# Optimization experiments

Hardware: AMD Instinct MI355X
Metric: run time of the kernel (lower is better)

## Reference

```python
import jax, jax.numpy as jnp
import numpy as np

B, S, D_MODEL, D_K, D_V = 4, 2048, 1024, 1024, 1024


def setup_inputs() -> dict:
    key = jax.random.key(0)
    k1, k2, k3, k4 = jax.random.split(key, 4)
    scale = 1.0 / np.sqrt(D_MODEL)
    x = jax.random.normal(k1, (B, S, D_MODEL), dtype=jnp.float32)
    Wq = jax.random.normal(k2, (D_K, D_MODEL), dtype=jnp.float32) * scale
    Wk = jax.random.normal(k3, (D_K, D_MODEL), dtype=jnp.float32) * scale
    Wv = jax.random.normal(k4, (D_V, D_MODEL), dtype=jnp.float32) * scale
    # causal mask: position i may attend to j <= i (True = keep)
    mask = jnp.broadcast_to(jnp.tril(jnp.ones((S, S), dtype=bool)), (B, S, S))
    return {"x": x, "mask": mask, "Wq": Wq, "Wk": Wk, "Wv": Wv}


def reference(x, mask, Wq, Wk, Wv):
    # nn.Linear(d, k, bias=False): y = x @ W.T with W of shape [k, d]
    q = jnp.einsum('bsd,kd->bsk', x, Wq)
    k = jnp.einsum('bsd,kd->bsk', x, Wk)
    v = jnp.einsum('bsd,vd->bsv', x, Wv)
    scores = jnp.einsum('bik,bjk->bij', q, k) / jnp.sqrt(jnp.float32(D_K))
    s = jnp.where(mask, scores, -jnp.inf)
    # masked, fully-masked-row-safe softmax (fully masked rows -> all zeros,
    # matching softmax[all-masked rows] = 0 in the original)
    m = jnp.max(s, axis=-1, keepdims=True)
    m_safe = jnp.where(jnp.isfinite(m), m, 0.0)
    e = jnp.exp(s - m_safe)          # exp(-inf) = 0 for masked entries
    denom = jnp.sum(e, axis=-1, keepdims=True)
    p = e / jnp.where(denom == 0.0, 1.0, denom)
    return jnp.einsum('bij,bjv->biv', p, v)
```

## Files before the change

### kernel.cpp

```cpp
#include <hip/hip_runtime.h>
#include <hip/hip_bf16.h>
#include <stdint.h>

#define SEQ   2048
#define DM    1024
#define NBAT  4

typedef __attribute__((ext_vector_type(8))) short  short8;
typedef __attribute__((ext_vector_type(4))) float  floatx4;

__device__ __forceinline__ unsigned short f2b(float f) {
    __hip_bfloat16 h = __float2bfloat16(f);
    unsigned short r;
    __builtin_memcpy(&r, &h, 2);
    return r;
}

__device__ __forceinline__ ushort4 pack4(float a, float b, float c, float d) {
    ushort4 u; u.x = f2b(a); u.y = f2b(b); u.z = f2b(c); u.w = f2b(d); return u;
}

__device__ __forceinline__ void gload16(const void* g, void* s) {
    __builtin_amdgcn_global_load_lds(
        (const __attribute__((address_space(1))) unsigned int*)(uintptr_t)g,
        (__attribute__((address_space(3))) unsigned int*)(uintptr_t)s,
        16, 0, 0);
}

__global__ void prep(const float4* __restrict__ x,
                     const float4* __restrict__ w0, const float4* __restrict__ w1,
                     const float4* __restrict__ w2,
                     ushort4* __restrict__ xb, ushort4* __restrict__ wall,
                     float* __restrict__ rsum)
{
    const int b = blockIdx.x;
    const int t = threadIdx.x;
    if (b < 8192) {
        const int i = b * 256 + t;
        float4 f = x[i];
        xb[i] = pack4(f.x, f.y, f.z, f.w);
    } else if (b < 11264) {
        const int idx  = b - 8192;
        const int wsel = idx >> 10;
        const int i    = (idx & 1023) * 256 + t;
        const float4* src = (wsel == 0) ? w0 : (wsel == 1) ? w1 : w2;
        float4 f = src[i];
        wall[(size_t)wsel * 262144 + i] = pack4(f.x, f.y, f.z, f.w);
    } else {
        rsum[(b - 11264) * 256 + t] = 0.f;
    }
}

template<int EPI>
__global__ __launch_bounds__(512, 2) void gemm256(
    const unsigned short* __restrict__ Ag, const unsigned short* __restrict__ Bg,
    void* __restrict__ P0, void* __restrict__ P1, void* __restrict__ P2,
    float* __restrict__ rowsum, float qscale)
{
    __shared__ __align__(16) unsigned short lds[65536];

    int m0, n0, ntl = 0, z = 0;
    const unsigned short* A;
    const unsigned short* Bm;

    if (EPI == 0) {
        const int bid = blockIdx.x;
        const int wg  = (bid & 7) * 48 + (bid >> 3);
        const int mt  = wg / 12; ntl = wg - mt * 12;
        m0 = mt * 256; n0 = ntl * 256;
        A = Ag; Bm = Bg;
    } else {
        z = blockIdx.z;
        const int f = blockIdx.x;
        int ti = (int)((sqrtf(8.f * f + 1.f) - 1.f) * 0.5f);
        while ((ti + 1) * (ti + 2) / 2 <= f) ti++;
        while (ti * (ti + 1) / 2 > f) ti--;
        const int tj = f - ti * (ti + 1) / 2;
        m0 = ti * 256; n0 = tj * 256;
        A = Ag + (size_t)z * SEQ * DM; Bm = Bg + (size_t)z * SEQ * DM;
    }

    const int t    = threadIdx.x;
    const int w    = t >> 6;
    const int lane = t & 63;
    const int wr   = w >> 2, wc = w & 3;
    const int r    = lane & 15, q = lane >> 4;

    const int srow = lane >> 3;
    const int scol = ((lane & 7) ^ srow) << 3;

    const int sk0 = ((0 + q) ^ (r & 7)) * 8;
    const int sk1 = ((4 + q) ^ (r & 7)) * 8;
    const int aRd = wr * 8192 + r * 64;
    const int bRd = 16384 + (wc >> 1) * 8192 + ((wc & 1) * 64 + r) * 64;

    floatx4 acc[8][4];
#pragma unroll
    for (int i = 0; i < 8; i++)
#pragma unroll
        for (int j = 0; j < 4; j++)
            acc[i][j] = (floatx4){0.f, 0.f, 0.f, 0.f};

#define STGC(G, R0, KB, CB) do { \
    gload16((G) + (size_t)((R0) + w * 16 + srow)     * DM + (KB) + scol, &lds[(CB) + w * 1024]); \
    gload16((G) + (size_t)((R0) + w * 16 + srow + 8) * DM + (KB) + scol, &lds[(CB) + w * 1024 + 512]); \
  } while (0)
#define STG4(KB, OB) do { \
    STGC(A,  m0,       (KB), (OB)); \
    STGC(A,  m0 + 128, (KB), (OB) + 8192); \
    STGC(Bm, n0,       (KB), (OB) + 16384); \
    STGC(Bm, n0 + 128, (KB), (OB) + 24576); \
  } while (0)

#define ONE_MFMA(AC, AF, BF) do { \
    if (EPI == 0) (AC) = __builtin_amdgcn_mfma_f32_16x16x32_bf16((AF), (BF), (AC), 0, 0, 0); \
    else          (AC) = __builtin_amdgcn_mfma_f32_16x16x32_bf16((BF), (AF), (AC), 0, 0, 0); \
  } while (0)

    STG4(0, 0);

    for (int tt = 0; tt < 16; ++tt) {
        const int cb  = (tt & 1) * 32768;
        const int ob  = 32768 - cb;
        const int nkb = (tt + 1 < 16 ? tt + 1 : 0) * 64;

        asm volatile("s_waitcnt vmcnt(0)" ::: "memory");
        __builtin_amdgcn_s_barrier();

        short8 a0[8], b0[4];
#pragma unroll
        for (int i = 0; i < 8; i++)
            a0[i] = *(const short8*)&lds[cb + aRd + i * 1024 + sk0];
#pragma unroll
        for (int j = 0; j < 4; j++)
            b0[j] = *(const short8*)&lds[cb + bRd + j * 1024 + sk0];

        STG4(nkb, ob);

        __builtin_amdgcn_s_setprio(1);
#pragma unroll
        for (int i = 0; i < 8; i++)
#pragma unroll
            for (int j = 0; j < 4; j++)
                ONE_MFMA(acc[i][j], a0[i], b0[j]);

        short8 a1[8], b1[4];
#pragma unroll
        for (int i = 0; i < 8; i++)
            a1[i] = *(const short8*)&lds[cb + aRd + i * 1024 + sk1];
#pragma unroll
        for (int j = 0; j < 4; j++)
            b1[j] = *(const short8*)&lds[cb + bRd + j * 1024 + sk1];
#pragma unroll
        for (int i = 0; i < 8; i++)
#pragma unroll
            for (int j = 0; j < 4; j++)
                ONE_MFMA(acc[i][j], a1[i], b1[j]);
        __builtin_amdgcn_s_setprio(0);
    }
#undef STGC
#undef STG4
#undef ONE_MFMA

    if (EPI == 0) {
        const int gmb = m0 + wr * 128 + q * 4;
        const int gnb = n0 + wc * 64 + r;
        unsigned short* Qo  = (unsigned short*)P0;
        unsigned short* Ko  = (unsigned short*)P1;
        unsigned short* Vto = (unsigned short*)P2;
        if (ntl < 4) {
#pragma unroll
            for (int i = 0; i < 8; i++) {
                const int gm = gmb + i * 16;
#pragma unroll
                for (int j = 0; j < 4; j++) {
                    const int gn = gnb + j * 16;
#pragma unroll
                    for (int rr = 0; rr < 4; rr++)
                        Qo[(size_t)(gm + rr) * 1024 + gn] = f2b(acc[i][j][rr] * qscale);
                }
            }
        } else if (ntl < 8) {
#pragma unroll
            for (int i = 0; i < 8; i++) {
                const int gm = gmb + i * 16;
#pragma unroll
                for (int j = 0; j < 4; j++) {
                    const int gn = gnb + j * 16;
#pragma unroll
                    for (int rr = 0; rr < 4; rr++)
                        Ko[(size_t)(gm + rr) * 1024 + (gn - 1024)] = f2b(acc[i][j][rr]);
                }
            }
        } else {
#pragma unroll
            for (int i = 0; i < 8; i++) {
                const int gm = gmb + i * 16;
                const int b  = gm >> 11;
                const int s  = gm & 2047;
#pragma unroll
                for (int j = 0; j < 4; j++) {
                    const int v = gnb + j * 16 - 2048;
                    *(ushort4*)&Vto[((size_t)(b * 1024 + v)) * 2048 + s] =
                        pack4(acc[i][j][0], acc[i][j][1], acc[i][j][2], acc[i][j][3]);
                }
            }
        }
    } else {
        const int gmb = m0 + wr * 128 + r;
        const int gnb = n0 + wc * 64 + q * 4;
        unsigned short* E = (unsigned short*)P0 + (size_t)z * SEQ * SEQ;
        float* rs = rowsum + (size_t)z * SEQ;
#pragma unroll
        for (int i = 0; i < 8; i++) {
            const int gm = gmb + i * 16;
            float part = 0.f;
#pragma unroll
            for (int j = 0; j < 4; j++) {
                const int gn = gnb + j * 16;
                float e0 = (gn + 0 <= gm) ? __expf(acc[i][j][0]) : 0.f;
                float e1 = (gn + 1 <= gm) ? __expf(acc[i][j][1]) : 0.f;
                float e2 = (gn + 2 <= gm) ? __expf(acc[i][j][2]) : 0.f;
                float e3 = (gn + 3 <= gm) ? __expf(acc[i][j][3]) : 0.f;
                part += (e0 + e1) + (e2 + e3);
                *(ushort4*)&E[(size_t)gm * SEQ + gn] = pack4(e0, e1, e2, e3);
            }
            part += __shfl_xor(part, 16, 64);
            part += __shfl_xor(part, 32, 64);
            if (q == 0) atomicAdd(&rs[gm], part);
        }
    }
}

#define SLOTS 24576

__global__ __launch_bounds__(512, 2) void attn_pv(
    const unsigned short* __restrict__ Ag, const unsigned short* __restrict__ Bg,
    float* __restrict__ Cv, const float* __restrict__ rowsum)
{
    __shared__ __align__(16) unsigned short lds[3 * SLOTS];

    const int z = blockIdx.z;
    const int m0 = (int)(gridDim.y - 1 - blockIdx.y) * 256;
    const int n0 = blockIdx.x * 128;

    const unsigned short* A  = Ag + (size_t)z * SEQ * SEQ;
    const unsigned short* Bm = Bg + (size_t)z * DM * SEQ;
    const int NT = (m0 + 256) / 64;

    const int t    = threadIdx.x;
    const int w    = t >> 6;
    const int lane = t & 63;
    const int wr   = w >> 1, wc = w & 1;
    const int r    = lane & 15, q = lane >> 4;

    const int srow = lane >> 3;
    const int scol = ((lane & 7) ^ srow) << 3;

    const int aoff = (wr >> 1) * 8192 + ((wr & 1) * 64 + r) * 64;
    const int boff = 16384 + (wc * 64 + r) * 64;
    const int sk0  = ((0 + q) ^ (r & 7)) * 8;
    const int sk1  = ((4 + q) ^ (r & 7)) * 8;

    floatx4 acc[4][4];
#pragma unroll
    for (int i = 0; i < 4; i++)
#pragma unroll
        for (int j = 0; j < 4; j++)
            acc[i][j] = (floatx4){0.f, 0.f, 0.f, 0.f};

#define ASTG(KB, SL) do { \
    gload16(A + (size_t)(m0 +       w * 16 + srow) * SEQ + (KB) + scol, &lds[(SL) +         w * 1024]); \
    gload16(A + (size_t)(m0 +   8 + w * 16 + srow) * SEQ + (KB) + scol, &lds[(SL) +         w * 1024 + 512]); \
    gload16(A + (size_t)(m0 + 128 + w * 16 + srow) * SEQ + (KB) + scol, &lds[(SL) + 8192 +  w * 1024]); \
    gload16(A + (size_t)(m0 + 136 + w * 16 + srow) * SEQ + (KB) + scol, &lds[(SL) + 8192 +  w * 1024 + 512]); \
  } while (0)
#define BSTG(KB, SL) do { \
    gload16(Bm + (size_t)(n0 +      w * 16 + srow) * SEQ + (KB) + scol, &lds[(SL) + 16384 + w * 1024]); \
    gload16(Bm + (size_t)(n0 +  8 + w * 16 + srow) * SEQ + (KB) + scol, &lds[(SL) + 16384 + w * 1024 + 512]); \
  } while (0)

    ASTG(0, 0);
    BSTG(0, 0);
    ASTG(64, SLOTS);
    BSTG(64, SLOTS);
    asm volatile("s_waitcnt vmcnt(6)" ::: "memory");
    __builtin_amdgcn_s_barrier();

    for (int tt = 0; tt < NT; ++tt) {
        const int sl  = (tt % 3) * SLOTS;
        const int nsl = ((tt + 2) % 3) * SLOTS;
        const int nkb = (tt + 2 < NT) ? (tt + 2) * 64 : 0;

        const int aB = sl + aoff;
        const int bB = sl + boff;
        short8 a00 = *(const short8*)&lds[aB + sk0 +    0];
        short8 a10 = *(const short8*)&lds[aB + sk0 + 1024];
        short8 a20 = *(const short8*)&lds[aB + sk0 + 2048];
        short8 a30 = *(const short8*)&lds[aB + sk0 + 3072];
        short8 b00 = *(const short8*)&lds[bB + sk0 +    0];
        short8 b10 = *(const short8*)&lds[bB + sk0 + 1024];
        short8 b20 = *(const short8*)&lds[bB + sk0 + 2048];
        short8 b30 = *(const short8*)&lds[bB + sk0 + 3072];
        short8 a01 = *(const short8*)&lds[aB + sk1 +    0];
        short8 a11 = *(const short8*)&lds[aB + sk1 + 1024];
        short8 a21 = *(const short8*)&lds[aB + sk1 + 2048];
        short8 a31 = *(const short8*)&lds[aB + sk1 + 3072];
        short8 b01 = *(const short8*)&lds[bB + sk1 +    0];
        short8 b11 = *(const short8*)&lds[bB + sk1 + 1024];
        short8 b21 = *(const short8*)&lds[bB + sk1 + 2048];
        short8 b31 = *(const short8*)&lds[bB + sk1 + 3072];

        ASTG(nkb, nsl);
        BSTG(nkb, nsl);
        asm volatile("s_waitcnt vmcnt(6)" ::: "memory");
        __builtin_amdgcn_s_barrier();

        __builtin_amdgcn_s_setprio(1);
        acc[0][0] = __builtin_amdgcn_mfma_f32_16x16x32_bf16(b00, a00, acc[0][0], 0, 0, 0);
        acc[0][1] = __builtin_amdgcn_mfma_f32_16x16x32_bf16(b10, a00, acc[0][1], 0, 0, 0);
        acc[0][2] = __builtin_amdgcn_mfma_f32_16x16x32_bf16(b20, a00, acc[0][2], 0, 0, 0);
        acc[0][3] = __builtin_amdgcn_mfma_f32_16x16x32_bf16(b30, a00, acc[0][3], 0, 0, 0);
        acc[1][0] = __builtin_amdgcn_mfma_f32_16x16x32_bf16(b00, a10, acc[1][0], 0, 0, 0);
        acc[1][1] = __builtin_amdgcn_mfma_f32_16x16x32_bf16(b10, a10, acc[1][1], 0, 0, 0);
        acc[1][2] = __builtin_amdgcn_mfma_f32_16x16x32_bf16(b20, a10, acc[1][2], 0, 0, 0);
        acc[1][3] = __builtin_amdgcn_mfma_f32_16x16x32_bf16(b30, a10, acc[1][3], 0, 0, 0);
        acc[2][0] = __builtin_amdgcn_mfma_f32_16x16x32_bf16(b00, a20, acc[2][0], 0, 0, 0);
        acc[2][1] = __builtin_amdgcn_mfma_f32_16x16x32_bf16(b10, a20, acc[2][1], 0, 0, 0);
        acc[2][2] = __builtin_amdgcn_mfma_f32_16x16x32_bf16(b20, a20, acc[2][2], 0, 0, 0);
        acc[2][3] = __builtin_amdgcn_mfma_f32_16x16x32_bf16(b30, a20, acc[2][3], 0, 0, 0);
        acc[3][0] = __builtin_amdgcn_mfma_f32_16x16x32_bf16(b00, a30, acc[3][0], 0, 0, 0);
        acc[3][1] = __builtin_amdgcn_mfma_f32_16x16x32_bf16(b10, a30, acc[3][1], 0, 0, 0);
        acc[3][2] = __builtin_amdgcn_mfma_f32_16x16x32_bf16(b20, a30, acc[3][2], 0, 0, 0);
        acc[3][3] = __builtin_amdgcn_mfma_f32_16x16x32_bf16(b30, a30, acc[3][3], 0, 0, 0);
        acc[0][0] = __builtin_amdgcn_mfma_f32_16x16x32_bf16(b01, a01, acc[0][0], 0, 0, 0);
        acc[0][1] = __builtin_amdgcn_mfma_f32_16x16x32_bf16(b11, a01, acc[0][1], 0, 0, 0);
        acc[0][2] = __builtin_amdgcn_mfma_f32_16x16x32_bf16(b21, a01, acc[0][2], 0, 0, 0);
        acc[0][3] = __builtin_amdgcn_mfma_f32_16x16x32_bf16(b31, a01, acc[0][3], 0, 0, 0);
        acc[1][0] = __builtin_amdgcn_mfma_f32_16x16x32_bf16(b01, a11, acc[1][0], 0, 0, 0);
        acc[1][1] = __builtin_amdgcn_mfma_f32_16x16x32_bf16(b11, a11, acc[1][1], 0, 0, 0);
        acc[1][2] = __builtin_amdgcn_mfma_f32_16x16x32_bf16(b21, a11, acc[1][2], 0, 0, 0);
        acc[1][3] = __builtin_amdgcn_mfma_f32_16x16x32_bf16(b31, a11, acc[1][3], 0, 0, 0);
        acc[2][0] = __builtin_amdgcn_mfma_f32_16x16x32_bf16(b01, a21, acc[2][0], 0, 0, 0);
        acc[2][1] = __builtin_amdgcn_mfma_f32_16x16x32_bf16(b11, a21, acc[2][1], 0, 0, 0);
        acc[2][2] = __builtin_amdgcn_mfma_f32_16x16x32_bf16(b21, a21, acc[2][2], 0, 0, 0);
        acc[2][3] = __builtin_amdgcn_mfma_f32_16x16x32_bf16(b31, a21, acc[2][3], 0, 0, 0);
        acc[3][0] = __builtin_amdgcn_mfma_f32_16x16x32_bf16(b01, a31, acc[3][0], 0, 0, 0);
        acc[3][1] = __builtin_amdgcn_mfma_f32_16x16x32_bf16(b11, a31, acc[3][1], 0, 0, 0);
        acc[3][2] = __builtin_amdgcn_mfma_f32_16x16x32_bf16(b21, a31, acc[3][2], 0, 0, 0);
        acc[3][3] = __builtin_amdgcn_mfma_f32_16x16x32_bf16(b31, a31, acc[3][3], 0, 0, 0);
        __builtin_amdgcn_s_setprio(0);
    }
#undef ASTG
#undef BSTG

    const int gmb = m0 + wr * 64 + r;
    const int gnb = n0 + wc * 64 + q * 4;
    float* C = Cv + (size_t)z * SEQ * DM;
    const float* rs = rowsum + (size_t)z * SEQ;
#pragma unroll
    for (int i = 0; i < 4; i++) {
        const int gm = gmb + i * 16;
        const float inv = 1.0f / rs[gm];
#pragma unroll
        for (int j = 0; j < 4; j++) {
            const int gn = gnb + j * 16;
            float4 o;
            o.x = acc[i][j][0] * inv;
            o.y = acc[i][j][1] * inv;
            o.z = acc[i][j][2] * inv;
            o.w = acc[i][j][3] * inv;
            *(float4*)&C[(size_t)gm * DM + gn] = o;
        }
    }
}

extern "C" void kernel_launch(void* const* d_in, const int* in_sizes, int n_in,
                              void* d_out, int out_size, void* d_ws, size_t ws_size,
                              hipStream_t stream) {
    (void)in_sizes; (void)n_in; (void)out_size; (void)ws_size;
    const float* x  = (const float*)d_in[0];
    const float* Wq = (const float*)d_in[2];
    const float* Wk = (const float*)d_in[3];
    const float* Wv = (const float*)d_in[4];

    char* base = (char*)d_ws;
    size_t off = 0;
    auto alloc = [&](size_t n) { char* p = base + off; off += (n + 255) & ~(size_t)255; return p; };

    unsigned short* xb   = (unsigned short*)alloc((size_t)NBAT * SEQ * DM * 2);
    unsigned short* wall = (unsigned short*)alloc((size_t)3 * DM * DM * 2);
    unsigned short* Qb   = (unsigned short*)alloc((size_t)NBAT * SEQ * DM * 2);
    unsigned short* Kb   = (unsigned short*)alloc((size_t)NBAT * SEQ * DM * 2);
    unsigned short* Vtb  = (unsigned short*)alloc((size_t)NBAT * DM * SEQ * 2);
    unsigned short* E    = (unsigned short*)alloc((size_t)NBAT * SEQ * SEQ * 2);
    float*          rsum = (float*)alloc((size_t)NBAT * SEQ * 4);

    prep<<<dim3(11296), dim3(256), 0, stream>>>(
        (const float4*)x, (const float4*)Wq, (const float4*)Wk, (const float4*)Wv,
        (ushort4*)xb, (ushort4*)wall, rsum);

    gemm256<0><<<dim3(384), dim3(512), 0, stream>>>(
        xb, wall, Qb, Kb, Vtb, nullptr, 0.03125f);

    gemm256<1><<<dim3(36, 1, NBAT), dim3(512), 0, stream>>>(
        Qb, Kb, E, nullptr, nullptr, rsum, 0.f);

    attn_pv<<<dim3(DM / 128, SEQ / 256, NBAT), dim3(512), 0, stream>>>(
        E, Vtb, (float*)d_out, rsum);
}
```

Measured before the change: 257.2 us.

## Restructure GEMM mainloop into triple-buffered K32 stages with split A/B loads

Replaces the double-buffered K=64 mainloop with a three-slot ring of K=32 stages (96KB LDS instead of 128KB). Each stage is split into two phases, and each phase issues loads for part of the next-next stage while running 16 MFMAs. A partial vmcnt wait replaces the full drain, so global loads stay in flight across barriers. The LDS swizzle and fragment layout are reworked to match. This trades more barriers and smaller MFMA batches per barrier for deeper prefetch and less LDS use, which may allow better occupancy.

```diff
diff --git a/kernel.cpp b/kernel.cpp
--- a/kernel.cpp
+++ b/kernel.cpp
@@ -52,12 +52,12 @@
 }
 
 template<int EPI>
-__global__ __launch_bounds__(512, 2) void gemm256(
+__global__ __launch_bounds__(512, 2) void gemmf(
     const unsigned short* __restrict__ Ag, const unsigned short* __restrict__ Bg,
     void* __restrict__ P0, void* __restrict__ P1, void* __restrict__ P2,
     float* __restrict__ rowsum, float qscale)
 {
-    __shared__ __align__(16) unsigned short lds[65536];
+    __shared__ __align__(16) unsigned short lds[49152];
 
     int m0, n0, ntl = 0, z = 0;
     const unsigned short* A;
@@ -86,13 +86,13 @@
     const int wr   = w >> 2, wc = w & 3;
     const int r    = lane & 15, q = lane >> 4;
 
-    const int srow = lane >> 3;
-    const int scol = ((lane & 7) ^ srow) << 3;
-
-    const int sk0 = ((0 + q) ^ (r & 7)) * 8;
-    const int sk1 = ((4 + q) ^ (r & 7)) * 8;
-    const int aRd = wr * 8192 + r * 64;
-    const int bRd = 16384 + (wc >> 1) * 8192 + ((wc & 1) * 64 + r) * 64;
+    const int slot8 = ((4 * (r & 1) + q) ^ ((r >> 1) & 7)) * 8;
+    const int aOff  = wr * 4096 + (r >> 1) * 64 + slot8;
+    const int bOff  = 8192 + wc * 2048 + (r >> 1) * 64 + slot8;
+
+    const int sx   = (t & 7) ^ ((t >> 3) & 7);
+    const int sRow = 2 * (t >> 3) + ((sx >> 2) & 1);
+    const int sK   = (sx & 3) * 8;
 
     floatx4 acc[8][4];
 #pragma unroll
@@ -101,15 +101,15 @@
         for (int j = 0; j < 4; j++)
             acc[i][j] = (floatx4){0.f, 0.f, 0.f, 0.f};
 
-#define STGC(G, R0, KB, CB) do { \
-    gload16((G) + (size_t)((R0) + w * 16 + srow)     * DM + (KB) + scol, &lds[(CB) + w * 1024]); \
-    gload16((G) + (size_t)((R0) + w * 16 + srow + 8) * DM + (KB) + scol, &lds[(CB) + w * 1024 + 512]); \
-  } while (0)
-#define STG4(KB, OB) do { \
-    STGC(A,  m0,       (KB), (OB)); \
-    STGC(A,  m0 + 128, (KB), (OB) + 8192); \
-    STGC(Bm, n0,       (KB), (OB) + 16384); \
-    STGC(Bm, n0 + 128, (KB), (OB) + 24576); \
+#define STG_A(H, SL) do { \
+    const int kb_ = (((H) < 32) ? (H) * 32 : 0) + sK; \
+    gload16(A + (((size_t)(m0 + sRow))       << 10) + kb_, &lds[(SL) * 16384 + w * 512]); \
+    gload16(A + (((size_t)(m0 + sRow + 128)) << 10) + kb_, &lds[(SL) * 16384 + w * 512 + 4096]); \
+  } while (0)
+#define STG_B(H, SL) do { \
+    const int kb_ = (((H) < 32) ? (H) * 32 : 0) + sK; \
+    gload16(Bm + (((size_t)(n0 + sRow))       << 10) + kb_, &lds[(SL) * 16384 + 8192 + w * 512]); \
+    gload16(Bm + (((size_t)(n0 + sRow + 128)) << 10) + kb_, &lds[(SL) * 16384 + 8192 + w * 512 + 4096]); \
   } while (0)
 
 #define ONE_MFMA(AC, AF, BF) do { \
@@ -117,49 +117,53 @@
     else          (AC) = __builtin_amdgcn_mfma_f32_16x16x32_bf16((BF), (AF), (AC), 0, 0, 0); \
   } while (0)
 
-    STG4(0, 0);
-
-    for (int tt = 0; tt < 16; ++tt) {
-        const int cb  = (tt & 1) * 32768;
-        const int ob  = 32768 - cb;
-        const int nkb = (tt + 1 < 16 ? tt + 1 : 0) * 64;
-
-        asm volatile("s_waitcnt vmcnt(0)" ::: "memory");
-        __builtin_amdgcn_s_barrier();
-
-        short8 a0[8], b0[4];
-#pragma unroll
-        for (int i = 0; i < 8; i++)
-            a0[i] = *(const short8*)&lds[cb + aRd + i * 1024 + sk0];
-#pragma unroll
-        for (int j = 0; j < 4; j++)
-            b0[j] = *(const short8*)&lds[cb + bRd + j * 1024 + sk0];
-
-        STG4(nkb, ob);
-
-        __builtin_amdgcn_s_setprio(1);
-#pragma unroll
-        for (int i = 0; i < 8; i++)
-#pragma unroll
-            for (int j = 0; j < 4; j++)
-                ONE_MFMA(acc[i][j], a0[i], b0[j]);
-
-        short8 a1[8], b1[4];
-#pragma unroll
-        for (int i = 0; i < 8; i++)
-            a1[i] = *(const short8*)&lds[cb + aRd + i * 1024 + sk1];
-#pragma unroll
-        for (int j = 0; j < 4; j++)
-            b1[j] = *(const short8*)&lds[cb + bRd + j * 1024 + sk1];
-#pragma unroll
-        for (int i = 0; i < 8; i++)
-#pragma unroll
-            for (int j = 0; j < 4; j++)
-                ONE_MFMA(acc[i][j], a1[i], b1[j]);
-        __builtin_amdgcn_s_setprio(0);
-    }
-#undef STGC
-#undef STG4
+#define PHASE(SL, MS, STG_EXPR) do { \
+    asm volatile("s_waitcnt vmcnt(4)" ::: "memory"); \
+    __builtin_amdgcn_s_barrier(); \
+    const int ab = (SL) * 16384 + aOff + (MS) * 2048; \
+    const int bb = (SL) * 16384 + bOff; \
+    short8 af0 = *(const short8*)&lds[ab +    0]; \
+    short8 af1 = *(const short8*)&lds[ab +  512]; \
+    short8 af2 = *(const short8*)&lds[ab + 1024]; \
+    short8 af3 = *(const short8*)&lds[ab + 1536]; \
+    short8 bf0 = *(const short8*)&lds[bb +    0]; \
+    short8 bf1 = *(const short8*)&lds[bb +  512]; \
+    short8 bf2 = *(const short8*)&lds[bb + 1024]; \
+    short8 bf3 = *(const short8*)&lds[bb + 1536]; \
+    STG_EXPR; \
+    asm volatile("s_waitcnt lgkmcnt(0)" ::: "memory"); \
+    __builtin_amdgcn_sched_barrier(0); \
+    __builtin_amdgcn_s_setprio(1); \
+    ONE_MFMA(acc[(MS)*4+0][0], af0, bf0); ONE_MFMA(acc[(MS)*4+0][1], af0, bf1); \
+    ONE_MFMA(acc[(MS)*4+0][2], af0, bf2); ONE_MFMA(acc[(MS)*4+0][3], af0, bf3); \
+    ONE_MFMA(acc[(MS)*4+1][0], af1, bf0); ONE_MFMA(acc[(MS)*4+1][1], af1, bf1); \
+    ONE_MFMA(acc[(MS)*4+1][2], af1, bf2); ONE_MFMA(acc[(MS)*4+1][3], af1, bf3); \
+    ONE_MFMA(acc[(MS)*4+2][0], af2, bf0); ONE_MFMA(acc[(MS)*4+2][1], af2, bf1); \
+    ONE_MFMA(acc[(MS)*4+2][2], af2, bf2); ONE_MFMA(acc[(MS)*4+2][3], af2, bf3); \
+    ONE_MFMA(acc[(MS)*4+3][0], af3, bf0); ONE_MFMA(acc[(MS)*4+3][1], af3, bf1); \
+    ONE_MFMA(acc[(MS)*4+3][2], af3, bf2); ONE_MFMA(acc[(MS)*4+3][3], af3, bf3); \
+    __builtin_amdgcn_s_setprio(0); \
+  } while (0)
+
+    STG_A(0, 0);
+    STG_B(0, 0);
+    STG_A(1, 1);
+    STG_B(1, 1);
+
+    int s0 = 0;
+    for (int T = 0; T < 16; ++T) {
+        const int s1 = (s0 + 1 == 3) ? 0 : s0 + 1;
+        const int s2 = (s1 + 1 == 3) ? 0 : s1 + 1;
+        const int h2 = 2 * T + 2, h3 = 2 * T + 3;
+        PHASE(s0, 0, STG_A(h2, s2));
+        PHASE(s0, 1, STG_B(h2, s2));
+        PHASE(s1, 0, STG_A(h3, s0));
+        PHASE(s1, 1, STG_B(h3, s0));
+        s0 = s2;
+    }
+#undef PHASE
+#undef STG_A
+#undef STG_B
 #undef ONE_MFMA
 
     if (EPI == 0) {
@@ -400,10 +404,10 @@
         (const float4*)x, (const float4*)Wq, (const float4*)Wk, (const float4*)Wv,
         (ushort4*)xb, (ushort4*)wall, rsum);
 
-    gemm256<0><<<dim3(384), dim3(512), 0, stream>>>(
+    gemmf<0><<<dim3(384), dim3(512), 0, stream>>>(
         xb, wall, Qb, Kb, Vtb, nullptr, 0.03125f);
 
-    gemm256<1><<<dim3(36, 1, NBAT), dim3(512), 0, stream>>>(
+    gemmf<1><<<dim3(36, 1, NBAT), dim3(512), 0, stream>>>(
         Qb, Kb, E, nullptr, nullptr, rsum, 0.f);
 
     attn_pv<<<dim3(DM / 128, SEQ / 256, NBAT), dim3(512), 0, stream>>>(
```

After: 262.8 us. +2.2%, slower.

## Use single-buffered QKV projection GEMM kernel with smaller LDS for higher occupancy

Applied to the files above, without the earlier changes.

Replaces the templated gemm256 QKV projection with a dedicated kernel that uses a single 64 KB LDS buffer (32768 shorts) and launch bounds of 4 waves per SIMD instead of 2. The K loop loads a tile, syncs, runs MFMAs and syncs again, so there is no explicit double-buffer prefetch. The aim is to hide latency through more resident workgroups rather than software pipelining, at the cost of exposing global-load latency inside each block and tighter register limits that risk spills with 128 accumulator floats per thread.

```diff
diff --git a/kernel.cpp b/kernel.cpp
--- a/kernel.cpp
+++ b/kernel.cpp
@@ -48,6 +48,127 @@
         wall[(size_t)wsel * 262144 + i] = pack4(f.x, f.y, f.z, f.w);
     } else {
         rsum[(b - 11264) * 256 + t] = 0.f;
+    }
+}
+
+__global__ __launch_bounds__(512, 4) void qkv_sb(
+    const unsigned short* __restrict__ A, const unsigned short* __restrict__ Bm,
+    unsigned short* __restrict__ Qo, unsigned short* __restrict__ Ko,
+    unsigned short* __restrict__ Vto, float qscale)
+{
+    __shared__ __align__(16) unsigned short lds[32768];
+
+    const int bid = blockIdx.x;
+    const int wg  = (bid & 7) * 48 + (bid >> 3);
+    const int mt  = wg / 12, ntl = wg - mt * 12;
+    const int m0  = mt * 256, n0 = ntl * 256;
+
+    const int t    = threadIdx.x;
+    const int w    = t >> 6;
+    const int lane = t & 63;
+    const int wr   = w >> 2, wc = w & 3;
+    const int r    = lane & 15, q = lane >> 4;
+
+    const int srow = lane >> 3;
+    const int scol = ((lane & 7) ^ srow) << 3;
+
+    const int sk0 = ((0 + q) ^ (r & 7)) * 8;
+    const int sk1 = ((4 + q) ^ (r & 7)) * 8;
+    const int aRd = wr * 8192 + r * 64;
+    const int bRd = 16384 + (wc >> 1) * 8192 + ((wc & 1) * 64 + r) * 64;
+
+    floatx4 acc[8][4];
+#pragma unroll
+    for (int i = 0; i < 8; i++)
+#pragma unroll
+        for (int j = 0; j < 4; j++)
+            acc[i][j] = (floatx4){0.f, 0.f, 0.f, 0.f};
+
+#define STGC(G, R0, KB, CB) do { \
+    gload16((G) + (size_t)((R0) + w * 16 + srow)     * DM + (KB) + scol, &lds[(CB) + w * 1024]); \
+    gload16((G) + (size_t)((R0) + w * 16 + srow + 8) * DM + (KB) + scol, &lds[(CB) + w * 1024 + 512]); \
+  } while (0)
+
+    for (int tt = 0; tt < 16; ++tt) {
+        const int kb = tt * 64;
+        STGC(A,  m0,       kb, 0);
+        STGC(A,  m0 + 128, kb, 8192);
+        STGC(Bm, n0,       kb, 16384);
+        STGC(Bm, n0 + 128, kb, 24576);
+        __syncthreads();
+
+        short8 a0[8], b0[4];
+#pragma unroll
+        for (int i = 0; i < 8; i++)
+            a0[i] = *(const short8*)&lds[aRd + i * 1024 + sk0];
+#pragma unroll
+        for (int j = 0; j < 4; j++)
+            b0[j] = *(const short8*)&lds[bRd + j * 1024 + sk0];
+
+        __builtin_amdgcn_s_setprio(1);
+#pragma unroll
+        for (int i = 0; i < 8; i++)
+#pragma unroll
+            for (int j = 0; j < 4; j++)
+                acc[i][j] = __builtin_amdgcn_mfma_f32_16x16x32_bf16(a0[i], b0[j], acc[i][j], 0, 0, 0);
+
+        short8 a1[8], b1[4];
+#pragma unroll
+        for (int i = 0; i < 8; i++)
+            a1[i] = *(const short8*)&lds[aRd + i * 1024 + sk1];
+#pragma unroll
+        for (int j = 0; j < 4; j++)
+            b1[j] = *(const short8*)&lds[bRd + j * 1024 + sk1];
+#pragma unroll
+        for (int i = 0; i < 8; i++)
+#pragma unroll
+            for (int j = 0; j < 4; j++)
+                acc[i][j] = __builtin_amdgcn_mfma_f32_16x16x32_bf16(a1[i], b1[j], acc[i][j], 0, 0, 0);
+        __builtin_amdgcn_s_setprio(0);
+
+        __syncthreads();
+    }
+#undef STGC
+
+    const int gmb = m0 + wr * 128 + q * 4;
+    const int gnb = n0 + wc * 64 + r;
+    if (ntl < 4) {
+#pragma unroll
+        for (int i = 0; i < 8; i++) {
+            const int gm = gmb + i * 16;
+#pragma unroll
+            for (int j = 0; j < 4; j++) {
+                const int gn = gnb + j * 16;
+#pragma unroll
+                for (int rr = 0; rr < 4; rr++)
+                    Qo[(size_t)(gm + rr) * 1024 + gn] = f2b(acc[i][j][rr] * qscale);
+            }
+        }
+    } else if (ntl < 8) {
+#pragma unroll
+        for (int i = 0; i < 8; i++) {
+            const int gm = gmb + i * 16;
+#pragma unroll
+            for (int j = 0; j < 4; j++) {
+                const int gn = gnb + j * 16;
+#pragma unroll
+                for (int rr = 0; rr < 4; rr++)
+                    Ko[(size_t)(gm + rr) * 1024 + (gn - 1024)] = f2b(acc[i][j][rr]);
+            }
+        }
+    } else {
+#pragma unroll
+        for (int i = 0; i < 8; i++) {
+            const int gm = gmb + i * 16;
+            const int b  = gm >> 11;
+            const int s  = gm & 2047;
+#pragma unroll
+            for (int j = 0; j < 4; j++) {
+                const int v = gnb + j * 16 - 2048;
+                *(ushort4*)&Vto[((size_t)(b * 1024 + v)) * 2048 + s] =
+                    pack4(acc[i][j][0], acc[i][j][1], acc[i][j][2], acc[i][j][3]);
+            }
+        }
     }
 }
 
@@ -400,8 +521,8 @@
         (const float4*)x, (const float4*)Wq, (const float4*)Wk, (const float4*)Wv,
         (ushort4*)xb, (ushort4*)wall, rsum);
 
-    gemm256<0><<<dim3(384), dim3(512), 0, stream>>>(
-        xb, wall, Qb, Kb, Vtb, nullptr, 0.03125f);
+    qkv_sb<<<dim3(384), dim3(512), 0, stream>>>(
+        xb, wall, Qb, Kb, Vtb, 0.03125f);
 
     gemm256<1><<<dim3(36, 1, NBAT), dim3(512), 0, stream>>>(
         Qb, Kb, E, nullptr, nullptr, rsum, 0.f);
```

New measurement: 681.5 us. 165% more time.
